# Kernel tuning notes

Hardware: AMD Instinct MI355X
Metric: run time of the kernel (lower is better)

Reference implementation:

```python
import jax, jax.numpy as jnp
import numpy as np

DIM = 512
HEADS = 8
DIM_HEAD = 64
HIDDEN = HEADS * DIM_HEAD  # 512
SCALE = 8.0
EPS = 1e-12  # matches torch F.normalize default eps


def l2norm(t):
    # F.normalize(t, dim=-1): t / max(||t||, eps)
    n = jnp.linalg.norm(t, axis=-1, keepdims=True)
    return t / jnp.maximum(n, EPS)


def setup_inputs() -> dict:
    key = jax.random.key(0)
    ks = jax.random.split(key, 4)
    x = jax.random.normal(ks[0], (8, 2048, DIM), dtype=jnp.float32)
    g = jnp.ones((DIM,), dtype=jnp.float32)  # RMSNorm gain
    w_qkv = jax.random.normal(ks[1], (DIM, 3 * HIDDEN), dtype=jnp.float32) * (DIM ** -0.5)
    q_scale = jnp.ones((DIM_HEAD,), dtype=jnp.float32)
    k_scale = jnp.ones((DIM_HEAD,), dtype=jnp.float32)
    w_out = jax.random.normal(ks[2], (HIDDEN, DIM), dtype=jnp.float32) * (HIDDEN ** -0.5)
    return {"x": x, "g": g, "w_qkv": w_qkv, "q_scale": q_scale,
            "k_scale": k_scale, "w_out": w_out}


def reference(x, g, w_qkv, q_scale, k_scale, w_out):
    B, N, D = x.shape
    # RMSNorm (lucidrains style): F.normalize(x, -1) * g * sqrt(dim)
    xn = l2norm(x) * g * jnp.sqrt(jnp.float32(D))
    qkv = xn @ w_qkv  # [B, N, 3*HIDDEN]
    q, k, v = jnp.split(qkv, 3, axis=-1)
    # b n (h d) -> b h n d
    split_heads = lambda t: t.reshape(B, N, HEADS, DIM_HEAD).transpose(0, 2, 1, 3)
    q, k, v = map(split_heads, (q, k, v))
    q = l2norm(q) * q_scale
    k = l2norm(k) * k_scale
    sim = jnp.einsum('bhid,bhjd->bhij', q, k) * SCALE
    attn = jax.nn.softmax(sim, axis=-1)
    out = jnp.einsum('bhij,bhjd->bhid', attn, v)
    out = out.transpose(0, 2, 1, 3).reshape(B, N, HIDDEN)
    return out @ w_out
```

## Files before the change

### kernel.cpp

```cpp
#include <hip/hip_runtime.h>
#include <math.h>

#define B_ 8
#define N_ 2048
#define DIM 512
#define HEADS 8
#define DHEAD 64
#define TOKENS (B_ * N_)
#define SZ ((size_t)TOKENS * DIM)
#define SCALE_ 8.0f
#define EPS_ 1e-12f
#define SQRT_DIM 22.62741699796952f

typedef unsigned long long u64;
typedef __attribute__((ext_vector_type(8))) short s8v;
typedef __attribute__((ext_vector_type(16))) float f16v;

#define MFMA(a, b, c) __builtin_amdgcn_mfma_f32_32x32x16_bf16(a, b, c, 0, 0, 0)

__device__ __forceinline__ ushort f2bf(float f) {
    uint u = __float_as_uint(f);
    return (ushort)((u + 0x7FFFu + ((u >> 16) & 1u)) >> 16);
}
__device__ __forceinline__ float bf2f(ushort h) {
    return __uint_as_float(((uint)h) << 16);
}
__device__ __forceinline__ void split2(float x, ushort& h, ushort& l) {
    h = f2bf(x);
    l = f2bf(x - bf2f(h));
}
__device__ __forceinline__ void split4(float4 f, u64& h4, u64& l4) {
    ushort h0, h1, h2, h3, l0, l1, l2, l3;
    split2(f.x, h0, l0); split2(f.y, h1, l1);
    split2(f.z, h2, l2); split2(f.w, h3, l3);
    h4 = (u64)h0 | ((u64)h1 << 16) | ((u64)h2 << 32) | ((u64)h3 << 48);
    l4 = (u64)l0 | ((u64)l1 << 16) | ((u64)l2 << 32) | ((u64)l3 << 48);
}

union BF8 { u64 q[2]; ushort us[8]; s8v v; };

__device__ __forceinline__ int swz(int row, int col) {
    return row * 64 + (col ^ ((row & 15) << 2));
}

__global__ __launch_bounds__(256) void split_w_k(const float* __restrict__ W,
                                                 ushort* __restrict__ WThi,
                                                 ushort* __restrict__ WTlo,
                                                 int K, int N) {
    __shared__ float T[32][33];
    const int k0 = blockIdx.y * 32, n0 = blockIdx.x * 32;
    const int tr = threadIdx.x >> 5;
    const int tc = threadIdx.x & 31;
#pragma unroll
    for (int i = 0; i < 4; ++i)
        T[tr + 8 * i][tc] = W[(size_t)(k0 + tr + 8 * i) * N + n0 + tc];
    __syncthreads();
#pragma unroll
    for (int i = 0; i < 4; ++i) {
        const int n = tr + 8 * i;
        ushort h, l;
        split2(T[tc][n], h, l);
        WThi[(size_t)(n0 + n) * K + k0 + tc] = h;
        WTlo[(size_t)(n0 + n) * K + k0 + tc] = l;
    }
}

__global__ __launch_bounds__(256) void rmsnorm_k(const float* __restrict__ x,
                                                 const float* __restrict__ g,
                                                 ushort* __restrict__ xnhi,
                                                 ushort* __restrict__ xnlo) {
    const int wave = threadIdx.x >> 6;
    const int lane = threadIdx.x & 63;
    const size_t t = (size_t)blockIdx.x * 4 + wave;
    const float4* xp = (const float4*)(x + t * DIM + lane * 8);
    float4 v0 = xp[0], v1 = xp[1];
    float ss = v0.x * v0.x + v0.y * v0.y + v0.z * v0.z + v0.w * v0.w +
               v1.x * v1.x + v1.y * v1.y + v1.z * v1.z + v1.w * v1.w;
#pragma unroll
    for (int off = 32; off; off >>= 1) ss += __shfl_xor(ss, off);
    const float s = SQRT_DIM / fmaxf(sqrtf(ss), EPS_);
    const float4* gp = (const float4*)(g + lane * 8);
    float4 g0 = gp[0], g1 = gp[1];
    float ov[8] = {v0.x * s * g0.x, v0.y * s * g0.y, v0.z * s * g0.z,
                   v0.w * s * g0.w, v1.x * s * g1.x, v1.y * s * g1.y,
                   v1.z * s * g1.z, v1.w * s * g1.w};
    ushort h[8], l[8];
#pragma unroll
    for (int j = 0; j < 8; ++j) split2(ov[j], h[j], l[j]);
    uint4 H, L;
    H.x = (uint)h[0] | ((uint)h[1] << 16); H.y = (uint)h[2] | ((uint)h[3] << 16);
    H.z = (uint)h[4] | ((uint)h[5] << 16); H.w = (uint)h[6] | ((uint)h[7] << 16);
    L.x = (uint)l[0] | ((uint)l[1] << 16); L.y = (uint)l[2] | ((uint)l[3] << 16);
    L.z = (uint)l[4] | ((uint)l[5] << 16); L.w = (uint)l[6] | ((uint)l[7] << 16);
    *(uint4*)(xnhi + t * DIM + lane * 8) = H;
    *(uint4*)(xnlo + t * DIM + lane * 8) = L;
}

template <int MODE>
__global__ __launch_bounds__(256, 2) void mfma_gemm_k(
    const ushort* __restrict__ Ahi, const ushort* __restrict__ Alo,
    const ushort* __restrict__ Bhi, const ushort* __restrict__ Blo,
    float* __restrict__ out) {
    __shared__ __attribute__((aligned(16))) ushort Ah[128 * 36];
    __shared__ __attribute__((aligned(16))) ushort Al[128 * 36];
    __shared__ __attribute__((aligned(16))) ushort Bh[128 * 36];
    __shared__ __attribute__((aligned(16))) ushort Bl[128 * 36];
    const int row0 = blockIdx.y * 128;
    const int col0 = blockIdx.x * 128;
    const int tid = threadIdx.x;
    const int wv = tid >> 6;
    const int wy = wv >> 1, wx = wv & 1;
    const int lo5 = tid & 31;
    const int hi5 = (tid & 63) >> 5;
    const int sr = tid >> 1;
    const int sh = (tid & 1) * 16;

    f16v acc[2][2];
#pragma unroll
    for (int i = 0; i < 2; ++i)
#pragma unroll
        for (int j = 0; j < 2; ++j)
#pragma unroll
            for (int r = 0; r < 16; ++r) acc[i][j][r] = 0.0f;

    uint4 ra[2][2], rb[2][2];
    const size_t abase = (size_t)(row0 + sr) * DIM + sh;
    const size_t bbase = (size_t)(col0 + sr) * DIM + sh;
    ra[0][0] = *(const uint4*)(Ahi + abase);     ra[0][1] = *(const uint4*)(Ahi + abase + 8);
    ra[1][0] = *(const uint4*)(Alo + abase);     ra[1][1] = *(const uint4*)(Alo + abase + 8);
    rb[0][0] = *(const uint4*)(Bhi + bbase);     rb[0][1] = *(const uint4*)(Bhi + bbase + 8);
    rb[1][0] = *(const uint4*)(Blo + bbase);     rb[1][1] = *(const uint4*)(Blo + bbase + 8);

    const int sbase = sr * 36 + sh;
    for (int k0 = 0; k0 < DIM; k0 += 32) {
        __syncthreads();
        *(uint2*)&Ah[sbase]      = make_uint2(ra[0][0].x, ra[0][0].y);
        *(uint2*)&Ah[sbase + 4]  = make_uint2(ra[0][0].z, ra[0][0].w);
        *(uint2*)&Ah[sbase + 8]  = make_uint2(ra[0][1].x, ra[0][1].y);
        *(uint2*)&Ah[sbase + 12] = make_uint2(ra[0][1].z, ra[0][1].w);
        *(uint2*)&Al[sbase]      = make_uint2(ra[1][0].x, ra[1][0].y);
        *(uint2*)&Al[sbase + 4]  = make_uint2(ra[1][0].z, ra[1][0].w);
        *(uint2*)&Al[sbase + 8]  = make_uint2(ra[1][1].x, ra[1][1].y);
        *(uint2*)&Al[sbase + 12] = make_uint2(ra[1][1].z, ra[1][1].w);
        *(uint2*)&Bh[sbase]      = make_uint2(rb[0][0].x, rb[0][0].y);
        *(uint2*)&Bh[sbase + 4]  = make_uint2(rb[0][0].z, rb[0][0].w);
        *(uint2*)&Bh[sbase + 8]  = make_uint2(rb[0][1].x, rb[0][1].y);
        *(uint2*)&Bh[sbase + 12] = make_uint2(rb[0][1].z, rb[0][1].w);
        *(uint2*)&Bl[sbase]      = make_uint2(rb[1][0].x, rb[1][0].y);
        *(uint2*)&Bl[sbase + 4]  = make_uint2(rb[1][0].z, rb[1][0].w);
        *(uint2*)&Bl[sbase + 8]  = make_uint2(rb[1][1].x, rb[1][1].y);
        *(uint2*)&Bl[sbase + 12] = make_uint2(rb[1][1].z, rb[1][1].w);
        __syncthreads();
        if (k0 + 32 < DIM) {
            const size_t a2 = abase + k0 + 32, b2 = bbase + k0 + 32;
            ra[0][0] = *(const uint4*)(Ahi + a2); ra[0][1] = *(const uint4*)(Ahi + a2 + 8);
            ra[1][0] = *(const uint4*)(Alo + a2); ra[1][1] = *(const uint4*)(Alo + a2 + 8);
            rb[0][0] = *(const uint4*)(Bhi + b2); rb[0][1] = *(const uint4*)(Bhi + b2 + 8);
            rb[1][0] = *(const uint4*)(Blo + b2); rb[1][1] = *(const uint4*)(Blo + b2 + 8);
        }
#pragma unroll
        for (int ks = 0; ks < 2; ++ks) {
            s8v a_h[2], a_l[2], b_h[2], b_l[2];
#pragma unroll
            for (int rt = 0; rt < 2; ++rt) {
                const int off = (wy * 64 + rt * 32 + lo5) * 36 + ks * 16 + 8 * hi5;
                BF8 th, tl;
                th.q[0] = *(const u64*)&Ah[off]; th.q[1] = *(const u64*)&Ah[off + 4];
                tl.q[0] = *(const u64*)&Al[off]; tl.q[1] = *(const u64*)&Al[off + 4];
                a_h[rt] = th.v; a_l[rt] = tl.v;
            }
#pragma unroll
            for (int ct = 0; ct < 2; ++ct) {
                const int off = (wx * 64 + ct * 32 + lo5) * 36 + ks * 16 + 8 * hi5;
                BF8 th, tl;
                th.q[0] = *(const u64*)&Bh[off]; th.q[1] = *(const u64*)&Bh[off + 4];
                tl.q[0] = *(const u64*)&Bl[off]; tl.q[1] = *(const u64*)&Bl[off + 4];
                b_h[ct] = th.v; b_l[ct] = tl.v;
            }
#pragma unroll
            for (int rt = 0; rt < 2; ++rt)
#pragma unroll
                for (int ct = 0; ct < 2; ++ct) {
                    acc[rt][ct] = MFMA(a_h[rt], b_h[ct], acc[rt][ct]);
                    acc[rt][ct] = MFMA(a_l[rt], b_h[ct], acc[rt][ct]);
                    acc[rt][ct] = MFMA(a_h[rt], b_l[ct], acc[rt][ct]);
                }
        }
    }
#pragma unroll
    for (int rt = 0; rt < 2; ++rt)
#pragma unroll
        for (int ct = 0; ct < 2; ++ct) {
            const int c = col0 + wx * 64 + ct * 32 + lo5;
            if (MODE == 0) {
                const int which = c / 512;
                const int within = c % 512;
                const int h = within >> 6, d = within & 63;
                float* ob = out + (size_t)which * SZ;
#pragma unroll
                for (int r = 0; r < 16; ++r) {
                    const int m = row0 + wy * 64 + rt * 32 + (r & 3) + 8 * (r >> 2) + 4 * hi5;
                    const int b = m >> 11, n = m & 2047;
                    ob[(((size_t)b * HEADS + h) * N_ + n) * DHEAD + d] = acc[rt][ct][r];
                }
            } else {
#pragma unroll
                for (int r = 0; r < 16; ++r) {
                    const int m = row0 + wy * 64 + rt * 32 + (r & 3) + 8 * (r >> 2) + 4 * hi5;
                    out[(size_t)m * DIM + c] = acc[rt][ct][r];
                }
            }
        }
}

__global__ __launch_bounds__(256) void qknorm_k(float* __restrict__ buf,
                                                const float* __restrict__ scale) {
    const int wave = threadIdx.x >> 6;
    const int lane = threadIdx.x & 63;
    const size_t row = (size_t)blockIdx.x * 4 + wave;
    float v = buf[row * DHEAD + lane];
    float ss = v * v;
#pragma unroll
    for (int off = 32; off; off >>= 1) ss += __shfl_xor(ss, off);
    const float inv = 1.0f / fmaxf(sqrtf(ss), EPS_);
    buf[row * DHEAD + lane] = v * inv * scale[lane];
}

__global__ __launch_bounds__(256, 2) void attn_k(const float* __restrict__ q,
                                                 const float* __restrict__ k,
                                                 const float* __restrict__ v,
                                                 ushort* __restrict__ Ohi,
                                                 ushort* __restrict__ Olo) {
    __shared__ __attribute__((aligned(16))) ushort Khi[64 * 64];
    __shared__ __attribute__((aligned(16))) ushort Klo[64 * 64];
    __shared__ __attribute__((aligned(16))) ushort Vthi[64 * 64];
    __shared__ __attribute__((aligned(16))) ushort Vtlo[64 * 64];
    __shared__ __attribute__((aligned(16))) ushort Pbuf[4][32 * 64];

    const int bh = blockIdx.y;
    const int q0 = blockIdx.x * 128;
    const int tid = threadIdx.x;
    const int ws = tid >> 6;
    const int lo5 = tid & 31;
    const int hi5 = (tid & 63) >> 5;
    const size_t base = (size_t)bh * (N_ * DHEAD);
    const float* kbh = k + base;
    const float* vbh = v + base;

    const int qrow0 = q0 + ws * 32;
    const int qrow = qrow0 + lo5;
    s8v qh[4], ql[4];
#pragma unroll
    for (int s = 0; s < 4; ++s) {
        const float* qp = q + base + (size_t)qrow * DHEAD + 16 * s + 8 * hi5;
        float4 a = *(const float4*)qp;
        float4 b = *(const float4*)(qp + 4);
        float qv[8] = {a.x, a.y, a.z, a.w, b.x, b.y, b.z, b.w};
        BF8 hh, ll;
#pragma unroll
        for (int j = 0; j < 8; ++j) {
            ushort h, l;
            split2(qv[j] * SCALE_, h, l);
            hh.us[j] = h; ll.us[j] = l;
        }
        qh[s] = hh.v; ql[s] = ll.v;
    }

    f16v o0 = {0,0,0,0,0,0,0,0,0,0,0,0,0,0,0,0};
    f16v o1 = {0,0,0,0,0,0,0,0,0,0,0,0,0,0,0,0};
    float dsum[16];
#pragma unroll
    for (int r = 0; r < 16; ++r) dsum[r] = 0.0f;

    ushort* Pw = Pbuf[ws];

    float4 kreg[4], vreg[4];
#pragma unroll
    for (int u = 0; u < 4; ++u) {
        const int f = tid + 256 * u;
        kreg[u] = *(const float4*)(kbh + (size_t)f * 4);
        vreg[u] = *(const float4*)(vbh + (size_t)f * 4);
    }

    for (int kt = 0; kt < N_ / 64; ++kt) {
        __syncthreads();
#pragma unroll
        for (int u = 0; u < 4; ++u) {
            const int f = tid + 256 * u;
            const int key = f >> 4;
            const int dd = (f & 15) * 4;
            u64 kh4, kl4;
            split4(kreg[u], kh4, kl4);
            *(u64*)&Khi[swz(key, dd)] = kh4;
            *(u64*)&Klo[swz(key, dd)] = kl4;
            float vv[4] = {vreg[u].x, vreg[u].y, vreg[u].z, vreg[u].w};
#pragma unroll
            for (int c = 0; c < 4; ++c) {
                ushort vh, vl;
                split2(vv[c], vh, vl);
                const int idx = swz(dd + c, key);
                Vthi[idx] = vh; Vtlo[idx] = vl;
            }
        }
        __syncthreads();
        if (kt + 1 < N_ / 64) {
#pragma unroll
            for (int u = 0; u < 4; ++u) {
                const int f = tid + 256 * u;
                const size_t off = (size_t)(kt + 1) * (64 * DHEAD) + (size_t)f * 4;
                kreg[u] = *(const float4*)(kbh + off);
                vreg[u] = *(const float4*)(vbh + off);
            }
        }
        f16v s0 = {0,0,0,0,0,0,0,0,0,0,0,0,0,0,0,0};
        f16v s1 = {0,0,0,0,0,0,0,0,0,0,0,0,0,0,0,0};
#pragma unroll
        for (int s = 0; s < 4; ++s) {
            const int d0 = 16 * s + 8 * hi5;
            BF8 b0h, b0l, b1h, b1l;
            b0h.q[0] = *(const u64*)&Khi[swz(lo5, d0)];
            b0h.q[1] = *(const u64*)&Khi[swz(lo5, d0 + 4)];
            b0l.q[0] = *(const u64*)&Klo[swz(lo5, d0)];
            b0l.q[1] = *(const u64*)&Klo[swz(lo5, d0 + 4)];
            b1h.q[0] = *(const u64*)&Khi[swz(32 + lo5, d0)];
            b1h.q[1] = *(const u64*)&Khi[swz(32 + lo5, d0 + 4)];
            b1l.q[0] = *(const u64*)&Klo[swz(32 + lo5, d0)];
            b1l.q[1] = *(const u64*)&Klo[swz(32 + lo5, d0 + 4)];
            s0 = MFMA(qh[s], b0h.v, s0);
            s1 = MFMA(qh[s], b1h.v, s1);
            s0 = MFMA(ql[s], b0h.v, s0);
            s1 = MFMA(ql[s], b1h.v, s1);
            s0 = MFMA(qh[s], b0l.v, s0);
            s1 = MFMA(qh[s], b1l.v, s1);
        }
#pragma unroll
        for (int r = 0; r < 16; ++r) {
            const float p0 = __expf(fminf(s0[r], 50.0f));
            const float p1 = __expf(fminf(s1[r], 50.0f));
            const ushort h0 = f2bf(p0);
            const ushort h1 = f2bf(p1);
            dsum[r] += bf2f(h0) + bf2f(h1);
            const int qr = (r & 3) + 8 * (r >> 2) + 4 * hi5;
            Pw[swz(qr, lo5)] = h0;
            Pw[swz(qr, 32 + lo5)] = h1;
        }
        asm volatile("s_waitcnt lgkmcnt(0)" ::: "memory");
        __builtin_amdgcn_sched_barrier(0);
#pragma unroll
        for (int s = 0; s < 4; ++s) {
            const int koff = 16 * s + 8 * hi5;
            BF8 pah, v0h, v0l, v1h, v1l;
            pah.q[0] = *(const u64*)&Pw[swz(lo5, koff)];
            pah.q[1] = *(const u64*)&Pw[swz(lo5, koff + 4)];
            v0h.q[0] = *(const u64*)&Vthi[swz(lo5, koff)];
            v0h.q[1] = *(const u64*)&Vthi[swz(lo5, koff + 4)];
            v0l.q[0] = *(const u64*)&Vtlo[swz(lo5, koff)];
            v0l.q[1] = *(const u64*)&Vtlo[swz(lo5, koff + 4)];
            v1h.q[0] = *(const u64*)&Vthi[swz(32 + lo5, koff)];
            v1h.q[1] = *(const u64*)&Vthi[swz(32 + lo5, koff + 4)];
            v1l.q[0] = *(const u64*)&Vtlo[swz(32 + lo5, koff)];
            v1l.q[1] = *(const u64*)&Vtlo[swz(32 + lo5, koff + 4)];
            o0 = MFMA(pah.v, v0h.v, o0);
            o1 = MFMA(pah.v, v1h.v, o1);
            o0 = MFMA(pah.v, v0l.v, o0);
            o1 = MFMA(pah.v, v1l.v, o1);
        }
    }
#pragma unroll
    for (int r = 0; r < 16; ++r) {
#pragma unroll
        for (int off = 1; off < 32; off <<= 1)
            dsum[r] += __shfl_xor(dsum[r], off);
    }
    const int b = bh >> 3, hh = bh & 7;
#pragma unroll
    for (int r = 0; r < 16; ++r) {
        const int qr = (r & 3) + 8 * (r >> 2) + 4 * hi5;
        const float inv = 1.0f / dsum[r];
        const size_t rowb = ((size_t)b * N_ + qrow0 + qr) * DIM + hh * DHEAD;
        ushort h, l;
        split2(o0[r] * inv, h, l);
        Ohi[rowb + lo5] = h;      Olo[rowb + lo5] = l;
        split2(o1[r] * inv, h, l);
        Ohi[rowb + 32 + lo5] = h; Olo[rowb + 32 + lo5] = l;
    }
}

extern "C" void kernel_launch(void* const* d_in, const int* in_sizes, int n_in,
                              void* d_out, int out_size, void* d_ws, size_t ws_size,
                              hipStream_t stream) {
    const float* x       = (const float*)d_in[0];
    const float* g       = (const float*)d_in[1];
    const float* w_qkv   = (const float*)d_in[2];
    const float* q_scale = (const float*)d_in[3];
    const float* k_scale = (const float*)d_in[4];
    const float* w_out   = (const float*)d_in[5];
    float* out = (float*)d_out;

    if (ws_size < 4 * SZ * sizeof(float)) return;

    char* base = (char*)d_ws;
    ushort* xnhi = (ushort*)base;
    ushort* xnlo = (ushort*)(base + (size_t)16 * 1024 * 1024);
    float*  qb   = (float*)(base + (size_t)32 * 1024 * 1024);
    float*  kb   = (float*)(base + (size_t)64 * 1024 * 1024);
    float*  vb   = (float*)(base + (size_t)96 * 1024 * 1024);
    ushort* Ohi  = xnhi;
    ushort* Olo  = xnlo;
    ushort* wqh = (ushort*)d_out;
    ushort* wql = wqh + (size_t)1536 * 512;
    ushort* woh = (ushort*)(base + (size_t)96 * 1024 * 1024);
    ushort* wol = woh + (size_t)512 * 512;

    split_w_k<<<dim3(48, 16), 256, 0, stream>>>(w_qkv, wqh, wql, 512, 1536);
    rmsnorm_k<<<TOKENS / 4, 256, 0, stream>>>(x, g, xnhi, xnlo);
    mfma_gemm_k<0><<<dim3(12, TOKENS / 128), 256, 0, stream>>>(xnhi, xnlo, wqh, wql, qb);
    qknorm_k<<<(TOKENS * HEADS) / 4, 256, 0, stream>>>(qb, q_scale);
    qknorm_k<<<(TOKENS * HEADS) / 4, 256, 0, stream>>>(kb, k_scale);
    attn_k<<<dim3(N_ / 128, B_ * HEADS), 256, 0, stream>>>(qb, kb, vb, Ohi, Olo);
    split_w_k<<<dim3(16, 16), 256, 0, stream>>>(w_out, woh, wol, 512, 512);
    mfma_gemm_k<1><<<dim3(4, TOKENS / 128), 256, 0, stream>>>(Ohi, Olo, woh, wol, out);
}
```

Before: 624.3 us.

## Fuse QK l2norm and bf16 hi/lo split into QKV GEMM epilogue

```diff
diff --git a/kernel.cpp b/kernel.cpp
--- a/kernel.cpp
+++ b/kernel.cpp
@@ -11,6 +11,7 @@
 #define SCALE_ 8.0f
 #define EPS_ 1e-12f
 #define SQRT_DIM 22.62741699796952f
+#define MB16 ((size_t)16 * 1024 * 1024)
 
 typedef unsigned long long u64;
 typedef __attribute__((ext_vector_type(8))) short s8v;
@@ -29,18 +30,11 @@
     h = f2bf(x);
     l = f2bf(x - bf2f(h));
 }
-__device__ __forceinline__ void split4(float4 f, u64& h4, u64& l4) {
-    ushort h0, h1, h2, h3, l0, l1, l2, l3;
-    split2(f.x, h0, l0); split2(f.y, h1, l1);
-    split2(f.z, h2, l2); split2(f.w, h3, l3);
-    h4 = (u64)h0 | ((u64)h1 << 16) | ((u64)h2 << 32) | ((u64)h3 << 48);
-    l4 = (u64)l0 | ((u64)l1 << 16) | ((u64)l2 << 32) | ((u64)l3 << 48);
-}
 
 union BF8 { u64 q[2]; ushort us[8]; s8v v; };
 
-__device__ __forceinline__ int swz(int row, int col) {
-    return row * 64 + (col ^ ((row & 15) << 2));
+__device__ __forceinline__ int swz8(int row, int col) {
+    return row * 64 + (col ^ ((row & 7) << 3));
 }
 
 __global__ __launch_bounds__(256) void split_w_k(const float* __restrict__ W,
@@ -96,8 +90,261 @@
     *(uint4*)(xnlo + t * DIM + lane * 8) = L;
 }
 
-template <int MODE>
-__global__ __launch_bounds__(256, 2) void mfma_gemm_k(
+__global__ __launch_bounds__(256, 2) void qkv_gemm_k(
+    const ushort* __restrict__ Ahi, const ushort* __restrict__ Alo,
+    const ushort* __restrict__ Bhi, const ushort* __restrict__ Blo,
+    const float* __restrict__ q_scale, const float* __restrict__ k_scale,
+    ushort* __restrict__ qhi, ushort* __restrict__ qlo,
+    ushort* __restrict__ khi, ushort* __restrict__ klo,
+    ushort* __restrict__ vthi, ushort* __restrict__ vtlo) {
+    __shared__ __attribute__((aligned(16))) ushort Ah[128 * 36];
+    __shared__ __attribute__((aligned(16))) ushort Al[128 * 36];
+    __shared__ __attribute__((aligned(16))) ushort Bh[128 * 36];
+    __shared__ __attribute__((aligned(16))) ushort Bl[128 * 36];
+    const int row0 = blockIdx.y * 128;
+    const int col0 = blockIdx.x * 128;
+    const int tid = threadIdx.x;
+    const int wv = tid >> 6;
+    const int wy = wv >> 1, wx = wv & 1;
+    const int lo5 = tid & 31;
+    const int hi5 = (tid & 63) >> 5;
+    const int sr = tid >> 1;
+    const int sh = (tid & 1) * 16;
+
+    f16v acc[2][2];
+#pragma unroll
+    for (int i = 0; i < 2; ++i)
+#pragma unroll
+        for (int j = 0; j < 2; ++j)
+#pragma unroll
+            for (int r = 0; r < 16; ++r) acc[i][j][r] = 0.0f;
+
+    uint4 ra[2][2], rb[2][2];
+    const size_t abase = (size_t)(row0 + sr) * DIM + sh;
+    const size_t bbase = (size_t)(col0 + sr) * DIM + sh;
+    ra[0][0] = *(const uint4*)(Ahi + abase);  ra[0][1] = *(const uint4*)(Ahi + abase + 8);
+    ra[1][0] = *(const uint4*)(Alo + abase);  ra[1][1] = *(const uint4*)(Alo + abase + 8);
+    rb[0][0] = *(const uint4*)(Bhi + bbase);  rb[0][1] = *(const uint4*)(Bhi + bbase + 8);
+    rb[1][0] = *(const uint4*)(Blo + bbase);  rb[1][1] = *(const uint4*)(Blo + bbase + 8);
+
+    const int sbase = sr * 36 + sh;
+    for (int k0 = 0; k0 < DIM; k0 += 32) {
+        __syncthreads();
+        *(uint4*)&Ah[sbase] = ra[0][0]; *(uint4*)&Ah[sbase + 8] = ra[0][1];
+        *(uint4*)&Al[sbase] = ra[1][0]; *(uint4*)&Al[sbase + 8] = ra[1][1];
+        *(uint4*)&Bh[sbase] = rb[0][0]; *(uint4*)&Bh[sbase + 8] = rb[0][1];
+        *(uint4*)&Bl[sbase] = rb[1][0]; *(uint4*)&Bl[sbase + 8] = rb[1][1];
+        __syncthreads();
+        if (k0 + 32 < DIM) {
+            const size_t a2 = abase + k0 + 32, b2 = bbase + k0 + 32;
+            ra[0][0] = *(const uint4*)(Ahi + a2); ra[0][1] = *(const uint4*)(Ahi + a2 + 8);
+            ra[1][0] = *(const uint4*)(Alo + a2); ra[1][1] = *(const uint4*)(Alo + a2 + 8);
+            rb[0][0] = *(const uint4*)(Bhi + b2); rb[0][1] = *(const uint4*)(Bhi + b2 + 8);
+            rb[1][0] = *(const uint4*)(Blo + b2); rb[1][1] = *(const uint4*)(Blo + b2 + 8);
+        }
+#pragma unroll
+        for (int ks = 0; ks < 2; ++ks) {
+            s8v a_h[2], a_l[2], b_h[2], b_l[2];
+#pragma unroll
+            for (int rt = 0; rt < 2; ++rt) {
+                const int off = (wy * 64 + rt * 32 + lo5) * 36 + ks * 16 + 8 * hi5;
+                BF8 th, tl;
+                th.q[0] = *(const u64*)&Ah[off]; th.q[1] = *(const u64*)&Ah[off + 4];
+                tl.q[0] = *(const u64*)&Al[off]; tl.q[1] = *(const u64*)&Al[off + 4];
+                a_h[rt] = th.v; a_l[rt] = tl.v;
+            }
+#pragma unroll
+            for (int ct = 0; ct < 2; ++ct) {
+                const int off = (wx * 64 + ct * 32 + lo5) * 36 + ks * 16 + 8 * hi5;
+                BF8 th, tl;
+                th.q[0] = *(const u64*)&Bh[off]; th.q[1] = *(const u64*)&Bh[off + 4];
+                tl.q[0] = *(const u64*)&Bl[off]; tl.q[1] = *(const u64*)&Bl[off + 4];
+                b_h[ct] = th.v; b_l[ct] = tl.v;
+            }
+#pragma unroll
+            for (int rt = 0; rt < 2; ++rt)
+#pragma unroll
+                for (int ct = 0; ct < 2; ++ct) {
+                    acc[rt][ct] = MFMA(a_h[rt], b_h[ct], acc[rt][ct]);
+                    acc[rt][ct] = MFMA(a_l[rt], b_h[ct], acc[rt][ct]);
+                    acc[rt][ct] = MFMA(a_h[rt], b_l[ct], acc[rt][ct]);
+                }
+        }
+    }
+    const int c64 = col0 + wx * 64;
+    const int which = c64 >> 9;
+    const int h = (c64 & 511) >> 6;
+    if (which < 2) {
+        const float* sc = which ? k_scale : q_scale;
+        const float s0c = sc[lo5], s1c = sc[32 + lo5];
+        ushort* Dh = which ? khi : qhi;
+        ushort* Dl = which ? klo : qlo;
+        const float mul = which ? 1.0f : SCALE_;
+#pragma unroll
+        for (int rt = 0; rt < 2; ++rt)
+#pragma unroll
+            for (int r = 0; r < 16; ++r) {
+                float v0 = acc[rt][0][r], v1 = acc[rt][1][r];
+                float ss = v0 * v0 + v1 * v1;
+#pragma unroll
+                for (int off = 16; off; off >>= 1) ss += __shfl_xor(ss, off);
+                const float inv = mul / fmaxf(sqrtf(ss), EPS_);
+                v0 *= inv * s0c; v1 *= inv * s1c;
+                const int m = row0 + wy * 64 + rt * 32 + (r & 3) + 8 * (r >> 2) + 4 * hi5;
+                const int b = m >> 11, n = m & 2047;
+                const size_t rb_ = (((size_t)b * HEADS + h) * N_ + n) * DHEAD;
+                ushort hh, ll;
+                split2(v0, hh, ll); Dh[rb_ + lo5] = hh;      Dl[rb_ + lo5] = ll;
+                split2(v1, hh, ll); Dh[rb_ + 32 + lo5] = hh; Dl[rb_ + 32 + lo5] = ll;
+            }
+    } else {
+#pragma unroll
+        for (int rt = 0; rt < 2; ++rt)
+#pragma unroll
+            for (int r = 0; r < 16; ++r) {
+                const int m = row0 + wy * 64 + rt * 32 + (r & 3) + 8 * (r >> 2) + 4 * hi5;
+                const int b = m >> 11, n = m & 2047;
+                const size_t vbase = ((size_t)b * HEADS + h) * (DHEAD * (size_t)N_) + n;
+                ushort hh, ll;
+                split2(acc[rt][0][r], hh, ll);
+                vthi[vbase + (size_t)lo5 * N_] = hh;
+                vtlo[vbase + (size_t)lo5 * N_] = ll;
+                split2(acc[rt][1][r], hh, ll);
+                vthi[vbase + (size_t)(32 + lo5) * N_] = hh;
+                vtlo[vbase + (size_t)(32 + lo5) * N_] = ll;
+            }
+    }
+}
+
+__global__ __launch_bounds__(256, 3) void attn_k(
+    const ushort* __restrict__ qhi, const ushort* __restrict__ qlo,
+    const ushort* __restrict__ khi, const ushort* __restrict__ klo,
+    const ushort* __restrict__ vthi, const ushort* __restrict__ vtlo,
+    ushort* __restrict__ Ohi, ushort* __restrict__ Olo) {
+    __shared__ __attribute__((aligned(16))) ushort Kh[64 * 64];
+    __shared__ __attribute__((aligned(16))) ushort Kl[64 * 64];
+    __shared__ __attribute__((aligned(16))) ushort Vh[64 * 64];
+    __shared__ __attribute__((aligned(16))) ushort Vl[64 * 64];
+    __shared__ __attribute__((aligned(16))) ushort Pbuf[4][32 * 64];
+
+    const int bh = blockIdx.y;
+    const int q0 = blockIdx.x * 128;
+    const int tid = threadIdx.x;
+    const int ws = tid >> 6;
+    const int lo5 = tid & 31;
+    const int hi5 = (tid & 63) >> 5;
+    const size_t base = (size_t)bh * (N_ * DHEAD);
+    const ushort* khp = khi + base;
+    const ushort* klp = klo + base;
+    const ushort* vhp = vthi + base;
+    const ushort* vlp = vtlo + base;
+    const int srow = tid >> 2;
+    const int scc = (tid & 3) * 16;
+
+    const int qrow0 = q0 + ws * 32;
+    const size_t qbase = base + (size_t)(qrow0 + lo5) * DHEAD;
+    s8v qh[4], ql[4];
+#pragma unroll
+    for (int s = 0; s < 4; ++s) {
+        const int d0 = 16 * s + 8 * hi5;
+        qh[s] = *(const s8v*)(qhi + qbase + d0);
+        ql[s] = *(const s8v*)(qlo + qbase + d0);
+    }
+
+    f16v o0 = {0,0,0,0,0,0,0,0,0,0,0,0,0,0,0,0};
+    f16v o1 = {0,0,0,0,0,0,0,0,0,0,0,0,0,0,0,0};
+    float dsum[16];
+#pragma unroll
+    for (int r = 0; r < 16; ++r) dsum[r] = 0.0f;
+    ushort* Pw = Pbuf[ws];
+
+    uint4 pre[8];
+#define LDTILE(kt_)                                                            \
+    {                                                                          \
+        const size_t kr = (size_t)((kt_) * 64 + srow) * 64 + scc;              \
+        pre[0] = *(const uint4*)(khp + kr); pre[1] = *(const uint4*)(khp + kr + 8); \
+        pre[2] = *(const uint4*)(klp + kr); pre[3] = *(const uint4*)(klp + kr + 8); \
+        const size_t vr = (size_t)srow * N_ + (kt_) * 64 + scc;                \
+        pre[4] = *(const uint4*)(vhp + vr); pre[5] = *(const uint4*)(vhp + vr + 8); \
+        pre[6] = *(const uint4*)(vlp + vr); pre[7] = *(const uint4*)(vlp + vr + 8); \
+    }
+
+    LDTILE(0)
+    const int sb0 = swz8(srow, scc), sb1 = swz8(srow, scc + 8);
+    for (int kt = 0; kt < N_ / 64; ++kt) {
+        __syncthreads();
+        *(uint4*)&Kh[sb0] = pre[0]; *(uint4*)&Kh[sb1] = pre[1];
+        *(uint4*)&Kl[sb0] = pre[2]; *(uint4*)&Kl[sb1] = pre[3];
+        *(uint4*)&Vh[sb0] = pre[4]; *(uint4*)&Vh[sb1] = pre[5];
+        *(uint4*)&Vl[sb0] = pre[6]; *(uint4*)&Vl[sb1] = pre[7];
+        __syncthreads();
+        if (kt + 1 < N_ / 64) LDTILE(kt + 1)
+        f16v s0 = {0,0,0,0,0,0,0,0,0,0,0,0,0,0,0,0};
+        f16v s1 = {0,0,0,0,0,0,0,0,0,0,0,0,0,0,0,0};
+#pragma unroll
+        for (int s = 0; s < 4; ++s) {
+            const int d0 = 16 * s + 8 * hi5;
+            const s8v b0h = *(const s8v*)&Kh[swz8(lo5, d0)];
+            const s8v b0l = *(const s8v*)&Kl[swz8(lo5, d0)];
+            const s8v b1h = *(const s8v*)&Kh[swz8(32 + lo5, d0)];
+            const s8v b1l = *(const s8v*)&Kl[swz8(32 + lo5, d0)];
+            s0 = MFMA(qh[s], b0h, s0);
+            s1 = MFMA(qh[s], b1h, s1);
+            s0 = MFMA(ql[s], b0h, s0);
+            s1 = MFMA(ql[s], b1h, s1);
+            s0 = MFMA(qh[s], b0l, s0);
+            s1 = MFMA(qh[s], b1l, s1);
+        }
+#pragma unroll
+        for (int r = 0; r < 16; ++r) {
+            const float p0 = __expf(fminf(s0[r], 50.0f));
+            const float p1 = __expf(fminf(s1[r], 50.0f));
+            const ushort h0 = f2bf(p0);
+            const ushort h1 = f2bf(p1);
+            dsum[r] += bf2f(h0) + bf2f(h1);
+            const int qr = (r & 3) + 8 * (r >> 2) + 4 * hi5;
+            Pw[swz8(qr, lo5)] = h0;
+            Pw[swz8(qr, 32 + lo5)] = h1;
+        }
+        asm volatile("s_waitcnt lgkmcnt(0)" ::: "memory");
+        __builtin_amdgcn_sched_barrier(0);
+#pragma unroll
+        for (int s = 0; s < 4; ++s) {
+            const int koff = 16 * s + 8 * hi5;
+            BF8 pah;
+            pah.q[0] = *(const u64*)&Pw[swz8(lo5, koff)];
+            pah.q[1] = *(const u64*)&Pw[swz8(lo5, koff) + 4];
+            const s8v v0h = *(const s8v*)&Vh[swz8(lo5, koff)];
+            const s8v v0l = *(const s8v*)&Vl[swz8(lo5, koff)];
+            const s8v v1h = *(const s8v*)&Vh[swz8(32 + lo5, koff)];
+            const s8v v1l = *(const s8v*)&Vl[swz8(32 + lo5, koff)];
+            o0 = MFMA(pah.v, v0h, o0);
+            o1 = MFMA(pah.v, v1h, o1);
+            o0 = MFMA(pah.v, v0l, o0);
+            o1 = MFMA(pah.v, v1l, o1);
+        }
+    }
+#pragma unroll
+    for (int r = 0; r < 16; ++r) {
+#pragma unroll
+        for (int off = 1; off < 32; off <<= 1)
+            dsum[r] += __shfl_xor(dsum[r], off);
+    }
+    const int b = bh >> 3, hh = bh & 7;
+#pragma unroll
+    for (int r = 0; r < 16; ++r) {
+        const int qr = (r & 3) + 8 * (r >> 2) + 4 * hi5;
+        const float inv = 1.0f / dsum[r];
+        const size_t rowb = ((size_t)b * N_ + qrow0 + qr) * DIM + hh * DHEAD;
+        ushort h, l;
+        split2(o0[r] * inv, h, l);
+        Ohi[rowb + lo5] = h;      Olo[rowb + lo5] = l;
+        split2(o1[r] * inv, h, l);
+        Ohi[rowb + 32 + lo5] = h; Olo[rowb + 32 + lo5] = l;
+    }
+}
+
+__global__ __launch_bounds__(256, 2) void out_gemm_k(
     const ushort* __restrict__ Ahi, const ushort* __restrict__ Alo,
     const ushort* __restrict__ Bhi, const ushort* __restrict__ Blo,
     float* __restrict__ out) {
@@ -126,30 +373,18 @@
     uint4 ra[2][2], rb[2][2];
     const size_t abase = (size_t)(row0 + sr) * DIM + sh;
     const size_t bbase = (size_t)(col0 + sr) * DIM + sh;
-    ra[0][0] = *(const uint4*)(Ahi + abase);     ra[0][1] = *(const uint4*)(Ahi + abase + 8);
-    ra[1][0] = *(const uint4*)(Alo + abase);     ra[1][1] = *(const uint4*)(Alo + abase + 8);
-    rb[0][0] = *(const uint4*)(Bhi + bbase);     rb[0][1] = *(const uint4*)(Bhi + bbase + 8);
-    rb[1][0] = *(const uint4*)(Blo + bbase);     rb[1][1] = *(const uint4*)(Blo + bbase + 8);
+    ra[0][0] = *(const uint4*)(Ahi + abase);  ra[0][1] = *(const uint4*)(Ahi + abase + 8);
+    ra[1][0] = *(const uint4*)(Alo + abase);  ra[1][1] = *(const uint4*)(Alo + abase + 8);
+    rb[0][0] = *(const uint4*)(Bhi + bbase);  rb[0][1] = *(const uint4*)(Bhi + bbase + 8);
+    rb[1][0] = *(const uint4*)(Blo + bbase);  rb[1][1] = *(const uint4*)(Blo + bbase + 8);
 
     const int sbase = sr * 36 + sh;
     for (int k0 = 0; k0 < DIM; k0 += 32) {
         __syncthreads();
-        *(uint2*)&Ah[sbase]      = make_uint2(ra[0][0].x, ra[0][0].y);
-        *(uint2*)&Ah[sbase + 4]  = make_uint2(ra[0][0].z, ra[0][0].w);
-        *(uint2*)&Ah[sbase + 8]  = make_uint2(ra[0][1].x, ra[0][1].y);
-        *(uint2*)&Ah[sbase + 12] = make_uint2(ra[0][1].z, ra[0][1].w);
-        *(uint2*)&Al[sbase]      = make_uint2(ra[1][0].x, ra[1][0].y);
-        *(uint2*)&Al[sbase + 4]  = make_uint2(ra[1][0].z, ra[1][0].w);
-        *(uint2*)&Al[sbase + 8]  = make_uint2(ra[1][1].x, ra[1][1].y);
-        *(uint2*)&Al[sbase + 12] = make_uint2(ra[1][1].z, ra[1][1].w);
-        *(uint2*)&Bh[sbase]      = make_uint2(rb[0][0].x, rb[0][0].y);
-        *(uint2*)&Bh[sbase + 4]  = make_uint2(rb[0][0].z, rb[0][0].w);
-        *(uint2*)&Bh[sbase + 8]  = make_uint2(rb[0][1].x, rb[0][1].y);
-        *(uint2*)&Bh[sbase + 12] = make_uint2(rb[0][1].z, rb[0][1].w);
-        *(uint2*)&Bl[sbase]      = make_uint2(rb[1][0].x, rb[1][0].y);
-        *(uint2*)&Bl[sbase + 4]  = make_uint2(rb[1][0].z, rb[1][0].w);
-        *(uint2*)&Bl[sbase + 8]  = make_uint2(rb[1][1].x, rb[1][1].y);
-        *(uint2*)&Bl[sbase + 12] = make_uint2(rb[1][1].z, rb[1][1].w);
+        *(uint4*)&Ah[sbase] = ra[0][0]; *(uint4*)&Ah[sbase + 8] = ra[0][1];
+        *(uint4*)&Al[sbase] = ra[1][0]; *(uint4*)&Al[sbase + 8] = ra[1][1];
+        *(uint4*)&Bh[sbase] = rb[0][0]; *(uint4*)&Bh[sbase + 8] = rb[0][1];
+        *(uint4*)&Bl[sbase] = rb[1][0]; *(uint4*)&Bl[sbase + 8] = rb[1][1];
         __syncthreads();
         if (k0 + 32 < DIM) {
             const size_t a2 = abase + k0 + 32, b2 = bbase + k0 + 32;
@@ -192,198 +427,12 @@
 #pragma unroll
         for (int ct = 0; ct < 2; ++ct) {
             const int c = col0 + wx * 64 + ct * 32 + lo5;
-            if (MODE == 0) {
-                const int which = c / 512;
-                const int within = c % 512;
-                const int h = within >> 6, d = within & 63;
-                float* ob = out + (size_t)which * SZ;
-#pragma unroll
-                for (int r = 0; r < 16; ++r) {
-                    const int m = row0 + wy * 64 + rt * 32 + (r & 3) + 8 * (r >> 2) + 4 * hi5;
-                    const int b = m >> 11, n = m & 2047;
-                    ob[(((size_t)b * HEADS + h) * N_ + n) * DHEAD + d] = acc[rt][ct][r];
-                }
-            } else {
-#pragma unroll
-                for (int r = 0; r < 16; ++r) {
-                    const int m = row0 + wy * 64 + rt * 32 + (r & 3) + 8 * (r >> 2) + 4 * hi5;
-                    out[(size_t)m * DIM + c] = acc[rt][ct][r];
-                }
-            }
-        }
-}
-
-__global__ __launch_bounds__(256) void qknorm_k(float* __restrict__ buf,
-                                                const float* __restrict__ scale) {
-    const int wave = threadIdx.x >> 6;
-    const int lane = threadIdx.x & 63;
-    const size_t row = (size_t)blockIdx.x * 4 + wave;
-    float v = buf[row * DHEAD + lane];
-    float ss = v * v;
-#pragma unroll
-    for (int off = 32; off; off >>= 1) ss += __shfl_xor(ss, off);
-    const float inv = 1.0f / fmaxf(sqrtf(ss), EPS_);
-    buf[row * DHEAD + lane] = v * inv * scale[lane];
-}
-
-__global__ __launch_bounds__(256, 2) void attn_k(const float* __restrict__ q,
-                                                 const float* __restrict__ k,
-                                                 const float* __restrict__ v,
-                                                 ushort* __restrict__ Ohi,
-                                                 ushort* __restrict__ Olo) {
-    __shared__ __attribute__((aligned(16))) ushort Khi[64 * 64];
-    __shared__ __attribute__((aligned(16))) ushort Klo[64 * 64];
-    __shared__ __attribute__((aligned(16))) ushort Vthi[64 * 64];
-    __shared__ __attribute__((aligned(16))) ushort Vtlo[64 * 64];
-    __shared__ __attribute__((aligned(16))) ushort Pbuf[4][32 * 64];
-
-    const int bh = blockIdx.y;
-    const int q0 = blockIdx.x * 128;
-    const int tid = threadIdx.x;
-    const int ws = tid >> 6;
-    const int lo5 = tid & 31;
-    const int hi5 = (tid & 63) >> 5;
-    const size_t base = (size_t)bh * (N_ * DHEAD);
-    const float* kbh = k + base;
-    const float* vbh = v + base;
-
-    const int qrow0 = q0 + ws * 32;
-    const int qrow = qrow0 + lo5;
-    s8v qh[4], ql[4];
-#pragma unroll
-    for (int s = 0; s < 4; ++s) {
-        const float* qp = q + base + (size_t)qrow * DHEAD + 16 * s + 8 * hi5;
-        float4 a = *(const float4*)qp;
-        float4 b = *(const float4*)(qp + 4);
-        float qv[8] = {a.x, a.y, a.z, a.w, b.x, b.y, b.z, b.w};
-        BF8 hh, ll;
-#pragma unroll
-        for (int j = 0; j < 8; ++j) {
-            ushort h, l;
-            split2(qv[j] * SCALE_, h, l);
-            hh.us[j] = h; ll.us[j] = l;
-        }
-        qh[s] = hh.v; ql[s] = ll.v;
-    }
-
-    f16v o0 = {0,0,0,0,0,0,0,0,0,0,0,0,0,0,0,0};
-    f16v o1 = {0,0,0,0,0,0,0,0,0,0,0,0,0,0,0,0};
-    float dsum[16];
-#pragma unroll
-    for (int r = 0; r < 16; ++r) dsum[r] = 0.0f;
-
-    ushort* Pw = Pbuf[ws];
-
-    float4 kreg[4], vreg[4];
-#pragma unroll
-    for (int u = 0; u < 4; ++u) {
-        const int f = tid + 256 * u;
-        kreg[u] = *(const float4*)(kbh + (size_t)f * 4);
-        vreg[u] = *(const float4*)(vbh + (size_t)f * 4);
-    }
-
-    for (int kt = 0; kt < N_ / 64; ++kt) {
-        __syncthreads();
-#pragma unroll
-        for (int u = 0; u < 4; ++u) {
-            const int f = tid + 256 * u;
-            const int key = f >> 4;
-            const int dd = (f & 15) * 4;
-            u64 kh4, kl4;
-            split4(kreg[u], kh4, kl4);
-            *(u64*)&Khi[swz(key, dd)] = kh4;
-            *(u64*)&Klo[swz(key, dd)] = kl4;
-            float vv[4] = {vreg[u].x, vreg[u].y, vreg[u].z, vreg[u].w};
-#pragma unroll
-            for (int c = 0; c < 4; ++c) {
-                ushort vh, vl;
-                split2(vv[c], vh, vl);
-                const int idx = swz(dd + c, key);
-                Vthi[idx] = vh; Vtlo[idx] = vl;
-            }
-        }
-        __syncthreads();
-        if (kt + 1 < N_ / 64) {
-#pragma unroll
-            for (int u = 0; u < 4; ++u) {
-                const int f = tid + 256 * u;
-                const size_t off = (size_t)(kt + 1) * (64 * DHEAD) + (size_t)f * 4;
-                kreg[u] = *(const float4*)(kbh + off);
-                vreg[u] = *(const float4*)(vbh + off);
-            }
-        }
-        f16v s0 = {0,0,0,0,0,0,0,0,0,0,0,0,0,0,0,0};
-        f16v s1 = {0,0,0,0,0,0,0,0,0,0,0,0,0,0,0,0};
-#pragma unroll
-        for (int s = 0; s < 4; ++s) {
-            const int d0 = 16 * s + 8 * hi5;
-            BF8 b0h, b0l, b1h, b1l;
-            b0h.q[0] = *(const u64*)&Khi[swz(lo5, d0)];
-            b0h.q[1] = *(const u64*)&Khi[swz(lo5, d0 + 4)];
-            b0l.q[0] = *(const u64*)&Klo[swz(lo5, d0)];
-            b0l.q[1] = *(const u64*)&Klo[swz(lo5, d0 + 4)];
-            b1h.q[0] = *(const u64*)&Khi[swz(32 + lo5, d0)];
-            b1h.q[1] = *(const u64*)&Khi[swz(32 + lo5, d0 + 4)];
-            b1l.q[0] = *(const u64*)&Klo[swz(32 + lo5, d0)];
-            b1l.q[1] = *(const u64*)&Klo[swz(32 + lo5, d0 + 4)];
-            s0 = MFMA(qh[s], b0h.v, s0);
-            s1 = MFMA(qh[s], b1h.v, s1);
-            s0 = MFMA(ql[s], b0h.v, s0);
-            s1 = MFMA(ql[s], b1h.v, s1);
-            s0 = MFMA(qh[s], b0l.v, s0);
-            s1 = MFMA(qh[s], b1l.v, s1);
-        }
-#pragma unroll
-        for (int r = 0; r < 16; ++r) {
-            const float p0 = __expf(fminf(s0[r], 50.0f));
-            const float p1 = __expf(fminf(s1[r], 50.0f));
-            const ushort h0 = f2bf(p0);
-            const ushort h1 = f2bf(p1);
-            dsum[r] += bf2f(h0) + bf2f(h1);
-            const int qr = (r & 3) + 8 * (r >> 2) + 4 * hi5;
-            Pw[swz(qr, lo5)] = h0;
-            Pw[swz(qr, 32 + lo5)] = h1;
-        }
-        asm volatile("s_waitcnt lgkmcnt(0)" ::: "memory");
-        __builtin_amdgcn_sched_barrier(0);
-#pragma unroll
-        for (int s = 0; s < 4; ++s) {
-            const int koff = 16 * s + 8 * hi5;
-            BF8 pah, v0h, v0l, v1h, v1l;
-            pah.q[0] = *(const u64*)&Pw[swz(lo5, koff)];
-            pah.q[1] = *(const u64*)&Pw[swz(lo5, koff + 4)];
-            v0h.q[0] = *(const u64*)&Vthi[swz(lo5, koff)];
-            v0h.q[1] = *(const u64*)&Vthi[swz(lo5, koff + 4)];
-            v0l.q[0] = *(const u64*)&Vtlo[swz(lo5, koff)];
-            v0l.q[1] = *(const u64*)&Vtlo[swz(lo5, koff + 4)];
-            v1h.q[0] = *(const u64*)&Vthi[swz(32 + lo5, koff)];
-            v1h.q[1] = *(const u64*)&Vthi[swz(32 + lo5, koff + 4)];
-            v1l.q[0] = *(const u64*)&Vtlo[swz(32 + lo5, koff)];
-            v1l.q[1] = *(const u64*)&Vtlo[swz(32 + lo5, koff + 4)];
-            o0 = MFMA(pah.v, v0h.v, o0);
-            o1 = MFMA(pah.v, v1h.v, o1);
-            o0 = MFMA(pah.v, v0l.v, o0);
-            o1 = MFMA(pah.v, v1l.v, o1);
-        }
-    }
-#pragma unroll
-    for (int r = 0; r < 16; ++r) {
-#pragma unroll
-        for (int off = 1; off < 32; off <<= 1)
-            dsum[r] += __shfl_xor(dsum[r], off);
-    }
-    const int b = bh >> 3, hh = bh & 7;
-#pragma unroll
-    for (int r = 0; r < 16; ++r) {
-        const int qr = (r & 3) + 8 * (r >> 2) + 4 * hi5;
-        const float inv = 1.0f / dsum[r];
-        const size_t rowb = ((size_t)b * N_ + qrow0 + qr) * DIM + hh * DHEAD;
-        ushort h, l;
-        split2(o0[r] * inv, h, l);
-        Ohi[rowb + lo5] = h;      Olo[rowb + lo5] = l;
-        split2(o1[r] * inv, h, l);
-        Ohi[rowb + 32 + lo5] = h; Olo[rowb + 32 + lo5] = l;
-    }
+#pragma unroll
+            for (int r = 0; r < 16; ++r) {
+                const int m = row0 + wy * 64 + rt * 32 + (r & 3) + 8 * (r >> 2) + 4 * hi5;
+                out[(size_t)m * DIM + c] = acc[rt][ct][r];
+            }
+        }
 }
 
 extern "C" void kernel_launch(void* const* d_in, const int* in_sizes, int n_in,
@@ -397,27 +446,31 @@
     const float* w_out   = (const float*)d_in[5];
     float* out = (float*)d_out;
 
-    if (ws_size < 4 * SZ * sizeof(float)) return;
-
-    char* base = (char*)d_ws;
-    ushort* xnhi = (ushort*)base;
-    ushort* xnlo = (ushort*)(base + (size_t)16 * 1024 * 1024);
-    float*  qb   = (float*)(base + (size_t)32 * 1024 * 1024);
-    float*  kb   = (float*)(base + (size_t)64 * 1024 * 1024);
-    float*  vb   = (float*)(base + (size_t)96 * 1024 * 1024);
+    if (ws_size < 8 * MB16) return;
+
+    char* W = (char*)d_ws;
+    ushort* xnhi = (ushort*)W;
+    ushort* xnlo = (ushort*)(W + MB16);
+    ushort* qhi  = (ushort*)(W + 2 * MB16);
+    ushort* qlo  = (ushort*)(W + 3 * MB16);
+    ushort* khi  = (ushort*)(W + 4 * MB16);
+    ushort* klo  = (ushort*)(W + 5 * MB16);
+    ushort* vthi = (ushort*)(W + 6 * MB16);
+    ushort* vtlo = (ushort*)(W + 7 * MB16);
     ushort* Ohi  = xnhi;
     ushort* Olo  = xnlo;
     ushort* wqh = (ushort*)d_out;
     ushort* wql = wqh + (size_t)1536 * 512;
-    ushort* woh = (ushort*)(base + (size_t)96 * 1024 * 1024);
-    ushort* wol = woh + (size_t)512 * 512;
+    ushort* woh = qhi;
+    ushort* wol = qhi + (size_t)512 * 512;
 
     split_w_k<<<dim3(48, 16), 256, 0, stream>>>(w_qkv, wqh, wql, 512, 1536);
     rmsnorm_k<<<TOKENS / 4, 256, 0, stream>>>(x, g, xnhi, xnlo);
-    mfma_gemm_k<0><<<dim3(12, TOKENS / 128), 256, 0, stream>>>(xnhi, xnlo, wqh, wql, qb);
-    qknorm_k<<<(TOKENS * HEADS) / 4, 256, 0, stream>>>(qb, q_scale);
-    qknorm_k<<<(TOKENS * HEADS) / 4, 256, 0, stream>>>(kb, k_scale);
-    attn_k<<<dim3(N_ / 128, B_ * HEADS), 256, 0, stream>>>(qb, kb, vb, Ohi, Olo);
+    qkv_gemm_k<<<dim3(12, TOKENS / 128), 256, 0, stream>>>(
+        xnhi, xnlo, wqh, wql, q_scale, k_scale,
+        qhi, qlo, khi, klo, vthi, vtlo);
+    attn_k<<<dim3(N_ / 128, B_ * HEADS), 256, 0, stream>>>(
+        qhi, qlo, khi, klo, vthi, vtlo, Ohi, Olo);
     split_w_k<<<dim3(16, 16), 256, 0, stream>>>(w_out, woh, wol, 512, 512);
-    mfma_gemm_k<1><<<dim3(4, TOKENS / 128), 256, 0, stream>>>(Ohi, Olo, woh, wol, out);
-}
+    out_gemm_k<<<dim3(4, TOKENS / 128), 256, 0, stream>>>(Ohi, Olo, woh, wol, out);
+}
```

Measured after the change: 1.236 ms. 1.98x slower.
